# Optimization experiments

Measured on AMD Instinct MI355X. Metric: run time of the kernel, lower is better.

Reference implementation:

```python
import jax, jax.numpy as jnp
import numpy as np
from jax import lax

MARGIN = 0.2
NMAX = 1


def setup_inputs() -> dict:
    key = jax.random.key(0)
    k1, k2 = jax.random.split(key)
    N, D = 8192, 512
    imgs = jax.random.normal(k1, (N, D), dtype=jnp.float32)
    caps = jax.random.normal(k2, (N, D), dtype=jnp.float32)
    return {"imgs": imgs, "caps": caps}


def reference(imgs, caps):
    # scores[i, j] = <img_i, cap_j>  -> [N, N]
    scores = jnp.matmul(imgs, caps.T)
    diag = jnp.diagonal(scores)  # [N]
    s = scores - 2.0 * jnp.diag(diag)
    # top-nmax over columns (axis 0): hardest negative captions per caption slot
    max_c = lax.top_k(s.T, NMAX)[0].T  # [NMAX, N]
    # top-nmax over rows (axis 1): hardest negative images per image slot
    max_i = lax.top_k(s, NMAX)[0]      # [N, NMAX]
    neg_cap = jnp.sum(jnp.maximum(max_c + (MARGIN - diag)[None, :], 0.0))
    neg_img = jnp.sum(jnp.maximum(max_i + (MARGIN - diag)[:, None], 0.0))
    return neg_cap + neg_img
```

## Files before the change

kernel.cpp:

```cpp
#include <hip/hip_runtime.h>

#define N_ROWS 8192
#define DIM    512

typedef __attribute__((ext_vector_type(4))) float frag_cd;
typedef __attribute__((ext_vector_type(2))) long long v2ll;

__device__ __forceinline__ unsigned f2fp8(float x) {
    float a = fabsf(x);
    unsigned s = (__float_as_uint(x) >> 31) << 7;
    if (a < 0.015625f) return s;
    a = fminf(a, 448.f);
    unsigned u = __float_as_uint(a);
    u += 0x7FFFFu + ((u >> 20) & 1u);
    unsigned exp = (u >> 23) - 120u;
    unsigned mant = (u >> 20) & 7u;
    return s | (exp << 3) | mant;
}
__device__ __forceinline__ unsigned pack4fp8(float4 v) {
    return f2fp8(v.x) | (f2fp8(v.y) << 8) | (f2fp8(v.z) << 16) | (f2fp8(v.w) << 24);
}
__device__ __forceinline__ unsigned enc_f32(float f) {
    unsigned u = __float_as_uint(f);
    return (u & 0x80000000u) ? ~u : (u | 0x80000000u);
}
__device__ __forceinline__ float dec_f32(unsigned k) {
    return __uint_as_float((k & 0x80000000u) ? (k & 0x7FFFFFFFu) : ~k);
}


__global__ __launch_bounds__(256) void k_prep(const float* __restrict__ imgs,
                                              const float* __restrict__ caps,
                                              unsigned char* __restrict__ fimgs,
                                              unsigned char* __restrict__ fcaps,
                                              float* __restrict__ diag,
                                              unsigned* __restrict__ rowmax,
                                              unsigned* __restrict__ colmax,
                                              float* __restrict__ out) {
    const int cr = blockIdx.x;
    const int t  = threadIdx.x;
    const int w = t >> 6, l = t & 63;
    const int kp = l >> 3, cg = l & 3, par = (l >> 2) & 1;
    if (cr == 0 && t == 0) out[0] = 0.f;
    const size_t ubase = (size_t)cr * 8192 + kp * 1024 + cg * 256 + par * 8;
    float ps[4];
    #pragma unroll
    for (int i = 0; i < 4; ++i) {
        const int row = w + 4 * i;
        const float* ar = imgs + ((size_t)cr * 16 + row) * DIM + l * 8;
        const float* br = caps + ((size_t)cr * 16 + row) * DIM + l * 8;
        float4 a0 = *(const float4*)ar, a1 = *(const float4*)(ar + 4);
        float4 b0 = *(const float4*)br, b1 = *(const float4*)(br + 4);
        uint2 oa, ob;
        oa.x = pack4fp8(a0); oa.y = pack4fp8(a1);
        ob.x = pack4fp8(b0); ob.y = pack4fp8(b1);
        *(uint2*)(fimgs + ubase + row * 16) = oa;
        *(uint2*)(fcaps + ubase + row * 16) = ob;
        ps[i] = a0.x * b0.x + a0.y * b0.y + a0.z * b0.z + a0.w * b0.w
              + a1.x * b1.x + a1.y * b1.y + a1.z * b1.z + a1.w * b1.w;
    }
    #pragma unroll
    for (int i = 0; i < 4; ++i) {
        float s = ps[i];
        #pragma unroll
        for (int m = 1; m < 64; m <<= 1) s += __shfl_xor(s, m, 64);
        if (l == 0) {
            const int r = cr * 16 + w + 4 * i;
            diag[r] = s; rowmax[r] = 0u; colmax[r] = 0u;
        }
    }
}

__global__ __launch_bounds__(256, 6) void k_gemm(const unsigned char* __restrict__ A,
                                                 const unsigned char* __restrict__ B,
                                                 unsigned* __restrict__ rowmax,
                                                 unsigned* __restrict__ colmax) {
    __shared__ unsigned char sA[2][4096];
    __shared__ unsigned char sB[2][8192];
    const int tid = threadIdx.x;
    const int w = tid >> 6, lane = tid & 63;
    const int f = (int)blockIdx.x;
    const int jb = (f & 7) * 8 + ((f >> 3) & 7);
    const int ib = f >> 6;
    const int j0 = jb << 7, i0 = ib << 6;
    const int q = lane >> 4, l15 = lane & 15;
    const int wr = (w & 1) << 5, wc = (w >> 1) << 6;

    const unsigned char* Ab = A + (size_t)(i0 >> 4) * 8192 + lane * 16;
    const unsigned char* Bb = B + (size_t)(j0 >> 4) * 8192 + lane * 16;

    frag_cd acc[2][4] = {};

    auto stage = [&](int bi, int kp) {
        __builtin_amdgcn_global_load_lds(
            (const __attribute__((address_space(1))) unsigned int*)(Ab + (size_t)w * 8192 + kp * 1024),
            (__attribute__((address_space(3))) unsigned int*)(&sA[bi][(w << 10) + (lane << 4)]), 16, 0, 0);
        #pragma unroll
        for (int j = 0; j < 2; ++j) {
            const int s = 2 * w + j;
            __builtin_amdgcn_global_load_lds(
                (const __attribute__((address_space(1))) unsigned int*)(Bb + (size_t)s * 8192 + kp * 1024),
                (__attribute__((address_space(3))) unsigned int*)(&sB[bi][(s << 10) + (lane << 4)]), 16, 0, 0);
        }
    };

    stage(0, 0);
    __syncthreads();

    const int u16 = ((q << 4) + l15) << 4;

    #pragma unroll
    for (int kp = 0; kp < 8; ++kp) {
        const int cur = kp & 1, nxt = cur ^ 1;
        if (kp < 7) stage(nxt, kp + 1);

        v2ll af[2], bfr[4];
        #pragma unroll
        for (int r = 0; r < 2; ++r)
            af[r] = *(const v2ll*)(&sA[cur][((((w & 1) << 1) + r) << 10) + u16]);
        #pragma unroll
        for (int c = 0; c < 4; ++c)
            bfr[c] = *(const v2ll*)(&sB[cur][((((w >> 1) << 2) + c) << 10) + u16]);
        #pragma unroll
        for (int r = 0; r < 2; ++r)
            #pragma unroll
            for (int c = 0; c < 4; ++c)
                acc[r][c] = __builtin_amdgcn_mfma_f32_16x16x32_fp8_fp8(af[r][0], bfr[c][0], acc[r][c], 0, 0, 0);
        #pragma unroll
        for (int r = 0; r < 2; ++r)
            #pragma unroll
            for (int c = 0; c < 4; ++c)
                acc[r][c] = __builtin_amdgcn_mfma_f32_16x16x32_fp8_fp8(af[r][1], bfr[c][1], acc[r][c], 0, 0, 0);

        __syncthreads();
    }

    const bool dblk = ((i0 >> 7) == jb);
    #pragma unroll
    for (int r = 0; r < 2; ++r)
        #pragma unroll
        for (int c = 0; c < 4; ++c)
            #pragma unroll
            for (int g = 0; g < 4; ++g) {
                float fv = acc[r][c][g];
                const int gi = wr + (r << 4) + (q << 2) + g;
                const int gj = wc + (c << 4) + l15;
                if (dblk && (i0 + gi) == (j0 + gj)) fv = -fv;
                acc[r][c][g] = fv;
            }

    #pragma unroll
    for (int r = 0; r < 2; ++r)
        #pragma unroll
        for (int g = 0; g < 4; ++g) {
            float m = fmaxf(fmaxf(acc[r][0][g], acc[r][1][g]),
                            fmaxf(acc[r][2][g], acc[r][3][g]));
            m = fmaxf(m, __shfl_xor(m, 1, 64));
            m = fmaxf(m, __shfl_xor(m, 2, 64));
            m = fmaxf(m, __shfl_xor(m, 4, 64));
            m = fmaxf(m, __shfl_xor(m, 8, 64));
            if (l15 == 0)
                atomicMax(&rowmax[i0 + wr + (r << 4) + (q << 2) + g], enc_f32(m));
        }
    #pragma unroll
    for (int c = 0; c < 4; ++c) {
        float m = acc[0][c][0];
        #pragma unroll
        for (int r = 0; r < 2; ++r)
            #pragma unroll
            for (int g = 0; g < 4; ++g) m = fmaxf(m, acc[r][c][g]);
        m = fmaxf(m, __shfl_xor(m, 16, 64));
        m = fmaxf(m, __shfl_xor(m, 32, 64));
        if (q == 0)
            atomicMax(&colmax[j0 + wc + (c << 4) + l15], enc_f32(m));
    }
}

__global__ __launch_bounds__(256) void k_final(const unsigned* __restrict__ rowmax,
                                               const unsigned* __restrict__ colmax,
                                               const float* __restrict__ diag,
                                               float* __restrict__ out) {
    const int idx = blockIdx.x * 256 + threadIdx.x;
    const float d = diag[idx];
    float s = fmaxf(dec_f32(rowmax[idx]) + 0.2f - d, 0.f)
            + fmaxf(dec_f32(colmax[idx]) + 0.2f - d, 0.f);
    #pragma unroll
    for (int m = 1; m < 64; m <<= 1) s += __shfl_xor(s, m, 64);
    __shared__ float red[4];
    if ((threadIdx.x & 63) == 0) red[threadIdx.x >> 6] = s;
    __syncthreads();
    if (threadIdx.x == 0)
        atomicAdd(out, red[0] + red[1] + red[2] + red[3]);
}

extern "C" void kernel_launch(void* const* d_in, const int* in_sizes, int n_in,
                              void* d_out, int out_size, void* d_ws, size_t ws_size,
                              hipStream_t stream) {
    const float* imgs = (const float*)d_in[0];
    const float* caps = (const float*)d_in[1];
    float* out = (float*)d_out;

    char* ws = (char*)d_ws;
    unsigned char* fimgs = (unsigned char*)ws;
    unsigned char* fcaps = (unsigned char*)(ws + 4194304);
    float*    diag   = (float*)   (ws + 8388608);
    unsigned* rowmax = (unsigned*)(ws + 8388608 + 32768);
    unsigned* colmax = (unsigned*)(ws + 8388608 + 65536);

    k_prep<<<N_ROWS / 16, 256, 0, stream>>>(imgs, caps, fimgs, fcaps,
                                            diag, rowmax, colmax, out);
    k_gemm<<<8192, 256, 0, stream>>>(fimgs, fcaps, rowmax, colmax);
    k_final<<<N_ROWS / 256, 256, 0, stream>>>(rowmax, colmax, diag, out);
}
```

Baseline: 155.4 us.

## Make GEMM kernel persistent and prefetch next tile during epilogue

Replaces the 8192-block GEMM launch with a persistent grid of 1024 blocks that loop over tiles with a stride of the grid size. The first k-slice of the next tile is staged into LDS while the current tile's masking, shuffle reductions and atomicMax epilogue run. The aim is to remove per-block launch and prologue cost and hide global-load latency behind the epilogue. In exchange the tile-to-block mapping changes, and the grid may not fill all CUs evenly at the chosen size and occupancy.

```diff
diff --git a/kernel.cpp b/kernel.cpp
--- a/kernel.cpp
+++ b/kernel.cpp
@@ -2,6 +2,7 @@
 
 #define N_ROWS 8192
 #define DIM    512
+#define GRID_GEMM 1024
 
 typedef __attribute__((ext_vector_type(4))) float frag_cd;
 typedef __attribute__((ext_vector_type(2))) long long v2ll;
@@ -79,100 +80,118 @@
     __shared__ unsigned char sB[2][8192];
     const int tid = threadIdx.x;
     const int w = tid >> 6, lane = tid & 63;
-    const int f = (int)blockIdx.x;
-    const int jb = (f & 7) * 8 + ((f >> 3) & 7);
-    const int ib = f >> 6;
-    const int j0 = jb << 7, i0 = ib << 6;
     const int q = lane >> 4, l15 = lane & 15;
     const int wr = (w & 1) << 5, wc = (w >> 1) << 6;
-
-    const unsigned char* Ab = A + (size_t)(i0 >> 4) * 8192 + lane * 16;
-    const unsigned char* Bb = B + (size_t)(j0 >> 4) * 8192 + lane * 16;
-
-    frag_cd acc[2][4] = {};
-
-    auto stage = [&](int bi, int kp) {
+    const int u16 = ((q << 4) + l15) << 4;
+
+    auto stage = [&](int bi, int kp, const unsigned char* Ap, const unsigned char* Bp) {
         __builtin_amdgcn_global_load_lds(
-            (const __attribute__((address_space(1))) unsigned int*)(Ab + (size_t)w * 8192 + kp * 1024),
+            (const __attribute__((address_space(1))) unsigned int*)(Ap + (size_t)w * 8192 + kp * 1024),
             (__attribute__((address_space(3))) unsigned int*)(&sA[bi][(w << 10) + (lane << 4)]), 16, 0, 0);
         #pragma unroll
         for (int j = 0; j < 2; ++j) {
             const int s = 2 * w + j;
             __builtin_amdgcn_global_load_lds(
-                (const __attribute__((address_space(1))) unsigned int*)(Bb + (size_t)s * 8192 + kp * 1024),
+                (const __attribute__((address_space(1))) unsigned int*)(Bp + (size_t)s * 8192 + kp * 1024),
                 (__attribute__((address_space(3))) unsigned int*)(&sB[bi][(s << 10) + (lane << 4)]), 16, 0, 0);
         }
     };
 
-    stage(0, 0);
-    __syncthreads();
-
-    const int u16 = ((q << 4) + l15) << 4;
-
-    #pragma unroll
-    for (int kp = 0; kp < 8; ++kp) {
-        const int cur = kp & 1, nxt = cur ^ 1;
-        if (kp < 7) stage(nxt, kp + 1);
-
-        v2ll af[2], bfr[4];
+    int job = (int)blockIdx.x;
+    int jb = (job & 7) * 8 + ((job >> 3) & 7);
+    int ib = job >> 6;
+    int j0 = jb << 7, i0 = ib << 6;
+    const unsigned char* Ab = A + (size_t)(i0 >> 4) * 8192 + lane * 16;
+    const unsigned char* Bb = B + (size_t)(j0 >> 4) * 8192 + lane * 16;
+
+    stage(0, 0, Ab, Bb);
+
+    for (;;) {
+        __syncthreads();
+
+        frag_cd acc[2][4] = {};
+        #pragma unroll
+        for (int kp = 0; kp < 8; ++kp) {
+            const int cur = kp & 1, nxt = cur ^ 1;
+            if (kp < 7) stage(nxt, kp + 1, Ab, Bb);
+
+            v2ll af[2], bfr[4];
+            #pragma unroll
+            for (int r = 0; r < 2; ++r)
+                af[r] = *(const v2ll*)(&sA[cur][((((w & 1) << 1) + r) << 10) + u16]);
+            #pragma unroll
+            for (int c = 0; c < 4; ++c)
+                bfr[c] = *(const v2ll*)(&sB[cur][((((w >> 1) << 2) + c) << 10) + u16]);
+            #pragma unroll
+            for (int r = 0; r < 2; ++r)
+                #pragma unroll
+                for (int c = 0; c < 4; ++c)
+                    acc[r][c] = __builtin_amdgcn_mfma_f32_16x16x32_fp8_fp8(af[r][0], bfr[c][0], acc[r][c], 0, 0, 0);
+            #pragma unroll
+            for (int r = 0; r < 2; ++r)
+                #pragma unroll
+                for (int c = 0; c < 4; ++c)
+                    acc[r][c] = __builtin_amdgcn_mfma_f32_16x16x32_fp8_fp8(af[r][1], bfr[c][1], acc[r][c], 0, 0, 0);
+
+            if (kp < 7) __syncthreads();
+        }
+
+        const int njob = job + GRID_GEMM;
+        if (njob < 8192) {
+            const int njb = (njob & 7) * 8 + ((njob >> 3) & 7);
+            const int nib = njob >> 6;
+            const unsigned char* nAb = A + (size_t)((nib << 6) >> 4) * 8192 + lane * 16;
+            const unsigned char* nBb = B + (size_t)((njb << 7) >> 4) * 8192 + lane * 16;
+            stage(0, 0, nAb, nBb);
+        }
+
+        const bool dblk = ((i0 >> 7) == jb);
         #pragma unroll
         for (int r = 0; r < 2; ++r)
-            af[r] = *(const v2ll*)(&sA[cur][((((w & 1) << 1) + r) << 10) + u16]);
-        #pragma unroll
-        for (int c = 0; c < 4; ++c)
-            bfr[c] = *(const v2ll*)(&sB[cur][((((w >> 1) << 2) + c) << 10) + u16]);
+            #pragma unroll
+            for (int c = 0; c < 4; ++c)
+                #pragma unroll
+                for (int g = 0; g < 4; ++g) {
+                    float fv = acc[r][c][g];
+                    const int gi = wr + (r << 4) + (q << 2) + g;
+                    const int gj = wc + (c << 4) + l15;
+                    if (dblk && (i0 + gi) == (j0 + gj)) fv = -fv;
+                    acc[r][c][g] = fv;
+                }
+
         #pragma unroll
         for (int r = 0; r < 2; ++r)
             #pragma unroll
-            for (int c = 0; c < 4; ++c)
-                acc[r][c] = __builtin_amdgcn_mfma_f32_16x16x32_fp8_fp8(af[r][0], bfr[c][0], acc[r][c], 0, 0, 0);
-        #pragma unroll
-        for (int r = 0; r < 2; ++r)
-            #pragma unroll
-            for (int c = 0; c < 4; ++c)
-                acc[r][c] = __builtin_amdgcn_mfma_f32_16x16x32_fp8_fp8(af[r][1], bfr[c][1], acc[r][c], 0, 0, 0);
-
-        __syncthreads();
-    }
-
-    const bool dblk = ((i0 >> 7) == jb);
-    #pragma unroll
-    for (int r = 0; r < 2; ++r)
-        #pragma unroll
-        for (int c = 0; c < 4; ++c)
-            #pragma unroll
             for (int g = 0; g < 4; ++g) {
-                float fv = acc[r][c][g];
-                const int gi = wr + (r << 4) + (q << 2) + g;
-                const int gj = wc + (c << 4) + l15;
-                if (dblk && (i0 + gi) == (j0 + gj)) fv = -fv;
-                acc[r][c][g] = fv;
+                float m = fmaxf(fmaxf(acc[r][0][g], acc[r][1][g]),
+                                fmaxf(acc[r][2][g], acc[r][3][g]));
+                m = fmaxf(m, __shfl_xor(m, 1, 64));
+                m = fmaxf(m, __shfl_xor(m, 2, 64));
+                m = fmaxf(m, __shfl_xor(m, 4, 64));
+                m = fmaxf(m, __shfl_xor(m, 8, 64));
+                if (l15 == 0)
+                    atomicMax(&rowmax[i0 + wr + (r << 4) + (q << 2) + g], enc_f32(m));
             }
-
-    #pragma unroll
-    for (int r = 0; r < 2; ++r)
-        #pragma unroll
-        for (int g = 0; g < 4; ++g) {
-            float m = fmaxf(fmaxf(acc[r][0][g], acc[r][1][g]),
-                            fmaxf(acc[r][2][g], acc[r][3][g]));
-            m = fmaxf(m, __shfl_xor(m, 1, 64));
-            m = fmaxf(m, __shfl_xor(m, 2, 64));
-            m = fmaxf(m, __shfl_xor(m, 4, 64));
-            m = fmaxf(m, __shfl_xor(m, 8, 64));
-            if (l15 == 0)
-                atomicMax(&rowmax[i0 + wr + (r << 4) + (q << 2) + g], enc_f32(m));
-        }
-    #pragma unroll
-    for (int c = 0; c < 4; ++c) {
-        float m = acc[0][c][0];
-        #pragma unroll
-        for (int r = 0; r < 2; ++r)
-            #pragma unroll
-            for (int g = 0; g < 4; ++g) m = fmaxf(m, acc[r][c][g]);
-        m = fmaxf(m, __shfl_xor(m, 16, 64));
-        m = fmaxf(m, __shfl_xor(m, 32, 64));
-        if (q == 0)
-            atomicMax(&colmax[j0 + wc + (c << 4) + l15], enc_f32(m));
+        #pragma unroll
+        for (int c = 0; c < 4; ++c) {
+            float m = acc[0][c][0];
+            #pragma unroll
+            for (int r = 0; r < 2; ++r)
+                #pragma unroll
+                for (int g = 0; g < 4; ++g) m = fmaxf(m, acc[r][c][g]);
+            m = fmaxf(m, __shfl_xor(m, 16, 64));
+            m = fmaxf(m, __shfl_xor(m, 32, 64));
+            if (q == 0)
+                atomicMax(&colmax[j0 + wc + (c << 4) + l15], enc_f32(m));
+        }
+
+        if (njob >= 8192) break;
+        job = njob;
+        jb = (job & 7) * 8 + ((job >> 3) & 7);
+        ib = job >> 6;
+        j0 = jb << 7; i0 = ib << 6;
+        Ab = A + (size_t)(i0 >> 4) * 8192 + lane * 16;
+        Bb = B + (size_t)(j0 >> 4) * 8192 + lane * 16;
     }
 }
 
@@ -209,6 +228,6 @@
 
     k_prep<<<N_ROWS / 16, 256, 0, stream>>>(imgs, caps, fimgs, fcaps,
                                             diag, rowmax, colmax, out);
-    k_gemm<<<8192, 256, 0, stream>>>(fimgs, fcaps, rowmax, colmax);
+    k_gemm<<<GRID_GEMM, 256, 0, stream>>>(fimgs, fcaps, rowmax, colmax);
     k_final<<<N_ROWS / 256, 256, 0, stream>>>(rowmax, colmax, diag, out);
 }
```

Result: slower. 202.1 us (+30.1%).
